# Kernel tuning notes

Measured on AMD Instinct MI355X. Metric: run time of the kernel, lower is better.

## Reference

```python
import jax, jax.numpy as jnp
import numpy as np

# Module config (matches init_kwargs)
SHAPE = (96, 128, 128)   # (D, H, W)
NUM_LAYERS = 2
K, S, P, DIL = 3, 2, 1, 1  # kernel, stride, padding, dilation (dilation=1)


def _sparse_maxpool(feat, mask):
    """One SparseMaxPool3d layer on a densified sparse tensor.

    feat: [B, D, H, W, C] float, inactive sites hold dtype-min
    mask: [B, D, H, W, 1] float 0/1 activity mask
    Max is taken only over ACTIVE input sites in each window (spconv semantics);
    an output site is active iff any input in its window is active.
    """
    neg = jnp.finfo(feat.dtype).min
    window = (1, K, K, K, 1)
    strides = (1, S, S, S, 1)
    pad = [(0, 0), (P, P), (P, P), (P, P), (0, 0)]
    masked = jnp.where(mask > 0, feat, neg)
    pooled = jax.lax.reduce_window(masked, neg, jax.lax.max, window, strides, pad)
    mask_out = jax.lax.reduce_window(mask, jnp.array(0, feat.dtype).item() * 0.0,
                                     jax.lax.max, window, strides, pad)
    return pooled, mask_out


def setup_inputs() -> dict:
    key = jax.random.key(0)
    k1, k2, k3, k4, k5 = jax.random.split(key, 5)
    N, C, B = 200000, 32, 2
    D, H, W = SHAPE
    features = jax.random.normal(k1, (N, C), dtype=jnp.float32)
    b = jax.random.randint(k2, (N,), 0, B)
    z = jax.random.randint(k3, (N,), 0, D)
    y = jax.random.randint(k4, (N,), 0, H)
    x = jax.random.randint(k5, (N,), 0, W)
    coors = jnp.stack([b, z, y, x], axis=1).astype(jnp.int32)
    return {"features": features, "coors": coors, "batch_size": B}


def reference(features, coors, batch_size):
    D, H, W = SHAPE
    C = features.shape[1]
    b, z, y, x = coors[:, 0], coors[:, 1], coors[:, 2], coors[:, 3]
    neg = jnp.finfo(features.dtype).min
    # Densify the sparse tensor (duplicate coords resolved by max, inactive = -inf)
    dense = jnp.full((batch_size, D, H, W, C), neg, features.dtype)
    dense = dense.at[b, z, y, x].max(features)
    mask = jnp.zeros((batch_size, D, H, W, 1), features.dtype).at[b, z, y, x].set(1.0)
    for _ in range(NUM_LAYERS):
        dense, mask = _sparse_maxpool(dense, mask)
    # Equivalent of SparseConvTensor.dense(): inactive output sites are 0
    return jnp.where(mask > 0, dense, jnp.zeros((), features.dtype))
```

## Files before the change

### kernel.cpp

```cpp
#include <hip/hip_runtime.h>
#include <cfloat>
#include <cstdint>

#define B_    2
#define OD    24
#define OH    32
#define OW    32
#define NC    32
#define NBINS (B_ * OD * OH * OW)
#define RSTRIDE 16
#define OVF_CAP 100000
#define SCAN_T 1024
#define CHUNK  (NBINS / SCAN_T)

#define TZ 4
#define TY 4
#define TX 4
#define TCELLS (TZ*TY*TX)
#define NTZ (OD/TZ)
#define NTY (OH/TY)
#define NTX (OW/TX)
#define NTILES (B_*NTZ*NTY*NTX)
#define NBZ (TZ+1)
#define NBY (TY+1)
#define NBX (TX+1)
#define NB  (NBZ*NBY*NBX)
#define LIST_CAP 1792

__device__ __forceinline__ unsigned xform(float f) {
    unsigned u = __float_as_uint(f);
    return u ^ ((unsigned)((int)u >> 31) | 0x80000000u);
}
__device__ __forceinline__ float unxform(unsigned t) {
    return (t == 0u) ? 0.0f
           : __uint_as_float((t >> 31) ? (t ^ 0x80000000u) : ~t);
}

__device__ __forceinline__ void slow_apply(unsigned* sm_out, const float* feat,
                                           int rec, int fm, int cb) {
    unsigned idx = ((unsigned)rec) >> 8;
    for (int c2 = 0; c2 < NC; ++c2) {
        unsigned tvv = xform(feat[idx * NC + c2]);
#pragma unroll
        for (int k = 0; k < 8; ++k) {
            const int koff = ((k & 1) * (TY * TX) + ((k >> 1) & 1) * TX
                           + ((k >> 2) & 1)) * NC;
            if ((fm >> k) & 1) atomicMax(&sm_out[cb * NC + koff + c2], tvv);
        }
    }
}


__global__ __launch_bounds__(256) void k_bin(const int* __restrict__ coors,
                                             int* __restrict__ counts,
                                             int* __restrict__ records,
                                             int* __restrict__ ovf_n,
                                             int2* __restrict__ ovf, int N) {
    int i = blockIdx.x * blockDim.x + threadIdx.x;
    if (i >= N) return;
    int4 cc = reinterpret_cast<const int4*>(coors)[i];
    int bin = (((cc.x * OD + (cc.y >> 2)) * OH + (cc.z >> 2)) * OW + (cc.w >> 2));
    int mask = 0xFF;
    if (!(cc.y & 3)) mask &= 0x55;
    if (!(cc.z & 3)) mask &= 0x33;
    if (!(cc.w & 3)) mask &= 0x0F;
    int rec = (i << 8) | mask;
    int pos = atomicAdd(&counts[bin], 1);
    if (pos < RSTRIDE) {
        records[bin * RSTRIDE + pos] = rec;
    } else {
        int o = atomicAdd(ovf_n, 1);
        if (o < OVF_CAP) ovf[o] = make_int2(bin, rec);
    }
}


__global__ __launch_bounds__(512) void k_tile(const float* __restrict__ feat,
                                              const int* __restrict__ counts,
                                              const int* __restrict__ records,
                                              const int* __restrict__ ovf_n,
                                              const int2* __restrict__ ovf,
                                              float4* __restrict__ out4) {
    __shared__ unsigned sm_out[TCELLS * NC];
    __shared__ int2 list[LIST_CAP];
    __shared__ int sm_cursor;

    const int t   = (blockIdx.x & 7) * (NTILES / 8) + (blockIdx.x >> 3);
    const int tid = threadIdx.x;
    const int tx_ = t & (NTX - 1);
    const int ty_ = (t >> 3) & (NTY - 1);
    const int rest = t >> 6;
    const int b   = (rest >= NTZ) ? 1 : 0;
    const int tz_ = rest - b * NTZ;
    const int tz0 = tz_ * TZ, ty0 = ty_ * TY, tx0 = tx_ * TX;

    if (tid == 0) sm_cursor = 0;
    for (int v = tid; v < TCELLS * NC; v += 512) sm_out[v] = 0u;
    __syncthreads();

    if (tid < 4 * NB) {
        int bn  = tid >> 2;
        int sl  = tid & 3;
        int rz  = bn / (NBY * NBX);
        int rem = bn - rz * (NBY * NBX);
        int ry  = rem / NBX;
        int rx  = rem - ry * NBX;
        int bz = tz0 - 1 + rz, by = ty0 - 1 + ry, bx = tx0 - 1 + rx;
        if ((bz | by | bx) >= 0) {
            int bin = ((b * OD + bz) * OH + by) * OW + bx;
            int cnt = counts[bin]; if (cnt > RSTRIDE) cnt = RSTRIDE;
            int4 q = *(const int4*)(records + bin * RSTRIDE + sl * 4);
            int bi = rz - 1, bj = ry - 1, bl = rx - 1;
            int vm = 0xFF;
            if (bi < 0) vm &= 0xAA;  if (bi > TZ - 2) vm &= 0x55;
            if (bj < 0) vm &= 0xCC;  if (bj > TY - 2) vm &= 0x33;
            if (bl < 0) vm &= 0xF0;  if (bl > TX - 2) vm &= 0x0F;
            int cb = bi * (TY * TX) + bj * TX + bl;
            int rs0 = sl << 2;
            int f0 = (rs0 + 0 < cnt) ? (q.x & vm & 0xFF) : 0;
            int f1 = (rs0 + 1 < cnt) ? (q.y & vm & 0xFF) : 0;
            int f2 = (rs0 + 2 < cnt) ? (q.z & vm & 0xFF) : 0;
            int f3 = (rs0 + 3 < cnt) ? (q.w & vm & 0xFF) : 0;
            int nk = (f0 != 0) + (f1 != 0) + (f2 != 0) + (f3 != 0);
            if (nk) {
                int pos = atomicAdd(&sm_cursor, nk);
                if (f0) { if (pos < LIST_CAP) list[pos] = make_int2((q.x & ~0xFF) | f0, cb);
                          else slow_apply(sm_out, feat, q.x, f0, cb); ++pos; }
                if (f1) { if (pos < LIST_CAP) list[pos] = make_int2((q.y & ~0xFF) | f1, cb);
                          else slow_apply(sm_out, feat, q.y, f1, cb); ++pos; }
                if (f2) { if (pos < LIST_CAP) list[pos] = make_int2((q.z & ~0xFF) | f2, cb);
                          else slow_apply(sm_out, feat, q.z, f2, cb); ++pos; }
                if (f3) { if (pos < LIST_CAP) list[pos] = make_int2((q.w & ~0xFF) | f3, cb);
                          else slow_apply(sm_out, feat, q.w, f3, cb); ++pos; }
            }
        }
    }

    int on = *ovf_n;
    if (on > 0 && tid == 0) {
        if (on > OVF_CAP) on = OVF_CAP;
        for (int e = 0; e < on; ++e) {
            int2 ov = ovf[e];
            int bx = ov.x & (OW - 1);
            int by = (ov.x >> 5) & (OH - 1);
            int rest2 = ov.x >> 10;
            int bb = (rest2 >= OD) ? 1 : 0;
            int bz = rest2 - bb * OD;
            if (bb != b) continue;
            int rz = bz - (tz0 - 1), ry = by - (ty0 - 1), rx = bx - (tx0 - 1);
            if (rz < 0 || rz >= NBZ || ry < 0 || ry >= NBY || rx < 0 || rx >= NBX) continue;
            int bi = rz - 1, bj = ry - 1, bl = rx - 1;
            int vm = 0xFF;
            if (bi < 0) vm &= 0xAA;  if (bi > TZ - 2) vm &= 0x55;
            if (bj < 0) vm &= 0xCC;  if (bj > TY - 2) vm &= 0x33;
            if (bl < 0) vm &= 0xF0;  if (bl > TX - 2) vm &= 0x0F;
            int fm = ov.y & vm & 0xFF;
            if (fm) {
                int pos = atomicAdd(&sm_cursor, 1);
                if (pos < LIST_CAP)
                    list[pos] = make_int2((ov.y & ~0xFF) | fm,
                                          bi * (TY * TX) + bj * TX + bl);
            }
        }
    }
    __syncthreads();
    int total = sm_cursor; if (total > LIST_CAP) total = LIST_CAP;

    const int s = tid >> 5;
    const int c = tid & 31;

    for (int j0 = s; j0 < total; j0 += 128) {
        int2 e[8];
        unsigned tv[8];
#pragma unroll
        for (int u = 0; u < 8; ++u) {
            int j = j0 + 16 * u;
            e[u] = (j < total) ? list[j] : make_int2(0, 0);
        }
#pragma unroll
        for (int u = 0; u < 8; ++u)
            tv[u] = xform(feat[(((unsigned)e[u].x) >> 8) * NC + c]);
#pragma unroll
        for (int u = 0; u < 8; ++u) {
#pragma unroll
            for (int k = 0; k < 8; ++k) {
                const int koff = ((k & 1) * (TY * TX) + ((k >> 1) & 1) * TX
                               + ((k >> 2) & 1)) * NC + c;
                if ((e[u].x >> k) & 1) atomicMax(&sm_out[e[u].y * NC + koff], tv[u]);
            }
        }
    }
    __syncthreads();

    {
        const int cell = tid >> 3, quad = tid & 7;
        const int i = cell >> 4, jj = (cell >> 2) & 3, l = cell & 3;
        uint4 uv = *(const uint4*)&sm_out[cell * NC + quad * 4];
        float4 o;
        o.x = unxform(uv.x); o.y = unxform(uv.y);
        o.z = unxform(uv.z); o.w = unxform(uv.w);
        out4[(((size_t)(b * OD + tz0 + i) * OH + (ty0 + jj)) * OW
              + (tx0 + l)) * (NC / 4) + quad] = o;
    }
}


__global__ void k_hist(const int* __restrict__ coors, int* __restrict__ counts, int N) {
    int i = blockIdx.x * blockDim.x + threadIdx.x;
    if (i >= N) return;
    int4 cc = reinterpret_cast<const int4*>(coors)[i];
    int bin = (((cc.x * OD + (cc.y >> 2)) * OH + (cc.z >> 2)) * OW + (cc.w >> 2));
    atomicAdd(&counts[bin], 1);
}

__global__ void k_scan(const int* __restrict__ counts,
                       int2* __restrict__ binfo,
                       int* __restrict__ cursor) {
    __shared__ int lds[SCAN_T];
    int t = threadIdx.x;
    int base = t * CHUNK;
    int s = 0;
#pragma unroll
    for (int k = 0; k < CHUNK; ++k) s += counts[base + k];
    lds[t] = s;
    __syncthreads();
    for (int d = 1; d < SCAN_T; d <<= 1) {
        int v = (t >= d) ? lds[t - d] : 0;
        __syncthreads();
        lds[t] += v;
        __syncthreads();
    }
    int excl = (t == 0) ? 0 : lds[t - 1];
    for (int k = 0; k < CHUNK; ++k) {
        int i = base + k;
        int c = counts[i];
        binfo[i] = make_int2(excl, c);
        cursor[i] = excl;
        excl += c;
    }
}

__global__ void k_place(const int* __restrict__ coors, int* __restrict__ cursor,
                        int* __restrict__ records, int N) {
    int i = blockIdx.x * blockDim.x + threadIdx.x;
    if (i >= N) return;
    int4 cc = reinterpret_cast<const int4*>(coors)[i];
    int bin = (((cc.x * OD + (cc.y >> 2)) * OH + (cc.z >> 2)) * OW + (cc.w >> 2));
    int pos = atomicAdd(&cursor[bin], 1);
    records[pos] = (i << 6) | (cc.y & 3) | ((cc.z & 3) << 2) | ((cc.w & 3) << 4);
}

__global__ __launch_bounds__(256) void k_gather_fb(const float4* __restrict__ feat4,
                                                   const int2* __restrict__ binfo,
                                                   const int* __restrict__ records,
                                                   float4* __restrict__ out4, int N) {
    int tid  = blockIdx.x * blockDim.x + threadIdx.x;
    int wid  = tid >> 6;
    int lane = threadIdx.x & 63;
    int q    = lane >> 3;
    int cq   = lane & 7;

    int ox  = wid & (OW - 1);
    int oy  = (wid >> 5) & (OH - 1);
    int bzc = wid >> 10;
    int b   = (bzc >= OD) ? 1 : 0;
    int oz  = bzc - b * OD;

    int2 bi[8];
#pragma unroll
    for (int k = 0; k < 8; ++k) {
        const int lz = k & 1, ly = (k >> 1) & 1, lx = (k >> 2) & 1;
        int z2 = oz - lz, y2 = oy - ly, x2 = ox - lx;
        bool okbin = ((z2 | y2 | x2) >= 0);
        int bin = ((b * OD + z2) * OH + y2) * OW + x2;
        int2 v = binfo[okbin ? bin : 0];
        if (!okbin) { v.x = N; v.y = 0; }
        bi[k] = v;
    }

    int recs[8];
#pragma unroll
    for (int k = 0; k < 8; ++k) {
        int j = (q < bi[k].y) ? q : 0;
        recs[k] = records[bi[k].x + j];
    }

    float4 m = make_float4(-FLT_MAX, -FLT_MAX, -FLT_MAX, -FLT_MAX);
    int any = 0;
#pragma unroll
    for (int k = 0; k < 8; ++k) {
        int rec = recs[k];
        bool ok = (q < bi[k].y);
        if (k & 1) ok = ok && ((rec & 3)  != 0);
        if (k & 2) ok = ok && ((rec & 12) != 0);
        if (k & 4) ok = ok && ((rec & 48) != 0);
        if (ok) {
            float4 f = feat4[(rec >> 6) * (NC / 4) + cq];
            m.x = fmaxf(m.x, f.x); m.y = fmaxf(m.y, f.y);
            m.z = fmaxf(m.z, f.z); m.w = fmaxf(m.w, f.w);
            any = 1;
        }
    }

#pragma unroll
    for (int k = 0; k < 8; ++k) {
        for (int j0 = 8; j0 < bi[k].y; j0 += 8) {
            int j = j0 + q;
            bool ok = (j < bi[k].y);
            int rec = records[bi[k].x + (ok ? j : 0)];
            if (k & 1) ok = ok && ((rec & 3)  != 0);
            if (k & 2) ok = ok && ((rec & 12) != 0);
            if (k & 4) ok = ok && ((rec & 48) != 0);
            if (ok) {
                float4 f = feat4[(rec >> 6) * (NC / 4) + cq];
                m.x = fmaxf(m.x, f.x); m.y = fmaxf(m.y, f.y);
                m.z = fmaxf(m.z, f.z); m.w = fmaxf(m.w, f.w);
                any = 1;
            }
        }
    }

#pragma unroll
    for (int s = 8; s < 64; s <<= 1) {
        m.x = fmaxf(m.x, __shfl_xor(m.x, s, 64));
        m.y = fmaxf(m.y, __shfl_xor(m.y, s, 64));
        m.z = fmaxf(m.z, __shfl_xor(m.z, s, 64));
        m.w = fmaxf(m.w, __shfl_xor(m.w, s, 64));
    }
    bool active = (__ballot(any) != 0ULL);

    if (q == 0) {
        float4 z4 = make_float4(0.f, 0.f, 0.f, 0.f);
        out4[wid * (NC / 4) + cq] = active ? m : z4;
    }
}


extern "C" void kernel_launch(void* const* d_in, const int* in_sizes, int n_in,
                              void* d_out, int out_size, void* d_ws, size_t ws_size,
                              hipStream_t stream) {
    const float* feat  = (const float*)d_in[0];
    const int*   coors = (const int*)d_in[1];
    const int N = in_sizes[0] / NC;
    float* out = (float*)d_out;

    const size_t fast_ints = (size_t)NBINS + 8 + (size_t)NBINS * RSTRIDE
                           + 2ull * OVF_CAP;
    if (ws_size >= fast_ints * sizeof(int)) {
        int*  counts  = (int*)d_ws;
        int*  ovf_n   = counts + NBINS;
        int*  records = counts + NBINS + 8;
        int2* ovf     = (int2*)(records + (size_t)NBINS * RSTRIDE);

        hipMemsetAsync(counts, 0, (NBINS + 8) * sizeof(int), stream);
        k_bin<<<(N + 255) / 256, 256, 0, stream>>>(coors, counts, records,
                                                   ovf_n, ovf, N);
        k_tile<<<NTILES, 512, 0, stream>>>(feat, counts, records,
                                           ovf_n, (const int2*)ovf, (float4*)out);
    } else {
        int*  counts  = (int*)d_ws;
        int2* binfo   = (int2*)(counts + NBINS);
        int*  cursor  = (int*)(binfo + NBINS);
        int*  records = cursor + NBINS;

        hipMemsetAsync(counts, 0, NBINS * sizeof(int), stream);
        k_hist <<<(N + 255) / 256, 256, 0, stream>>>(coors, counts, N);
        k_scan <<<1, SCAN_T, 0, stream>>>(counts, binfo, cursor);
        k_place<<<(N + 255) / 256, 256, 0, stream>>>(coors, cursor, records, N);
        k_gather_fb<<<(NBINS * 64) / 256, 256, 0, stream>>>(
            (const float4*)feat, (const int2*)binfo, records, (float4*)out, N);
    }
}
```

Baseline: 41.26 us.

## Replace shared atomicMax scatter with per-cell index lists and register max gather

Rewrites the tile kernel's inner phase. Each input record is now expanded into per-output-cell index lists in shared memory (with a small shared overflow list) instead of one shared list with bitmasks. Each thread then computes the max for four cells over one channel in registers, replacing the per-channel shared atomicMax scatter and the float/uint ordering transform. The trade is more shared atomics during list building and uneven per-cell loop lengths in the gather phase.

```diff
diff --git a/kernel.cpp b/kernel.cpp
--- a/kernel.cpp
+++ b/kernel.cpp
@@ -16,7 +16,7 @@
 #define TZ 4
 #define TY 4
 #define TX 4
-#define TCELLS (TZ*TY*TX)
+#define TCELLS 64
 #define NTZ (OD/TZ)
 #define NTY (OH/TY)
 #define NTX (OW/TX)
@@ -25,30 +25,8 @@
 #define NBY (TY+1)
 #define NBX (TX+1)
 #define NB  (NBZ*NBY*NBX)
-#define LIST_CAP 1792
-
-__device__ __forceinline__ unsigned xform(float f) {
-    unsigned u = __float_as_uint(f);
-    return u ^ ((unsigned)((int)u >> 31) | 0x80000000u);
-}
-__device__ __forceinline__ float unxform(unsigned t) {
-    return (t == 0u) ? 0.0f
-           : __uint_as_float((t >> 31) ? (t ^ 0x80000000u) : ~t);
-}
-
-__device__ __forceinline__ void slow_apply(unsigned* sm_out, const float* feat,
-                                           int rec, int fm, int cb) {
-    unsigned idx = ((unsigned)rec) >> 8;
-    for (int c2 = 0; c2 < NC; ++c2) {
-        unsigned tvv = xform(feat[idx * NC + c2]);
-#pragma unroll
-        for (int k = 0; k < 8; ++k) {
-            const int koff = ((k & 1) * (TY * TX) + ((k >> 1) & 1) * TX
-                           + ((k >> 2) & 1)) * NC;
-            if ((fm >> k) & 1) atomicMax(&sm_out[cb * NC + koff + c2], tvv);
-        }
-    }
-}
+#define CELLCAP 64
+#define SOVF_CAP 1024
 
 
 __global__ __launch_bounds__(256) void k_bin(const int* __restrict__ coors,
@@ -74,16 +52,31 @@
     }
 }
 
+__device__ __forceinline__ void push_rec(int rec, int fm, int cb,
+                                         int* cellcnt, int* celllist,
+                                         int2* sovf, int* sovf_n) {
+    int idx = (int)(((unsigned)rec) >> 8);
+    while (fm) {
+        int k = __builtin_ctz(fm); fm &= fm - 1;
+        int cell = cb + ((k & 1) << 4) + (((k >> 1) & 1) << 2) + ((k >> 2) & 1);
+        int pos = atomicAdd(&cellcnt[cell], 1);
+        if (pos < CELLCAP) celllist[cell * CELLCAP + pos] = idx;
+        else { int o = atomicAdd(sovf_n, 1);
+               if (o < SOVF_CAP) sovf[o] = make_int2(cell, idx); }
+    }
+}
+
 
 __global__ __launch_bounds__(512) void k_tile(const float* __restrict__ feat,
                                               const int* __restrict__ counts,
                                               const int* __restrict__ records,
                                               const int* __restrict__ ovf_n,
                                               const int2* __restrict__ ovf,
-                                              float4* __restrict__ out4) {
-    __shared__ unsigned sm_out[TCELLS * NC];
-    __shared__ int2 list[LIST_CAP];
-    __shared__ int sm_cursor;
+                                              float* __restrict__ out) {
+    __shared__ int  cellcnt[TCELLS];
+    __shared__ int  celllist[TCELLS * CELLCAP];
+    __shared__ int2 sovf[SOVF_CAP];
+    __shared__ int  sovf_n;
 
     const int t   = (blockIdx.x & 7) * (NTILES / 8) + (blockIdx.x >> 3);
     const int tid = threadIdx.x;
@@ -94,8 +87,8 @@
     const int tz_ = rest - b * NTZ;
     const int tz0 = tz_ * TZ, ty0 = ty_ * TY, tx0 = tx_ * TX;
 
-    if (tid == 0) sm_cursor = 0;
-    for (int v = tid; v < TCELLS * NC; v += 512) sm_out[v] = 0u;
+    if (tid < TCELLS) cellcnt[tid] = 0;
+    if (tid == 0) sovf_n = 0;
     __syncthreads();
 
     if (tid < 4 * NB) {
@@ -121,18 +114,10 @@
             int f1 = (rs0 + 1 < cnt) ? (q.y & vm & 0xFF) : 0;
             int f2 = (rs0 + 2 < cnt) ? (q.z & vm & 0xFF) : 0;
             int f3 = (rs0 + 3 < cnt) ? (q.w & vm & 0xFF) : 0;
-            int nk = (f0 != 0) + (f1 != 0) + (f2 != 0) + (f3 != 0);
-            if (nk) {
-                int pos = atomicAdd(&sm_cursor, nk);
-                if (f0) { if (pos < LIST_CAP) list[pos] = make_int2((q.x & ~0xFF) | f0, cb);
-                          else slow_apply(sm_out, feat, q.x, f0, cb); ++pos; }
-                if (f1) { if (pos < LIST_CAP) list[pos] = make_int2((q.y & ~0xFF) | f1, cb);
-                          else slow_apply(sm_out, feat, q.y, f1, cb); ++pos; }
-                if (f2) { if (pos < LIST_CAP) list[pos] = make_int2((q.z & ~0xFF) | f2, cb);
-                          else slow_apply(sm_out, feat, q.z, f2, cb); ++pos; }
-                if (f3) { if (pos < LIST_CAP) list[pos] = make_int2((q.w & ~0xFF) | f3, cb);
-                          else slow_apply(sm_out, feat, q.w, f3, cb); ++pos; }
-            }
+            if (f0) push_rec(q.x, f0, cb, cellcnt, celllist, sovf, &sovf_n);
+            if (f1) push_rec(q.y, f1, cb, cellcnt, celllist, sovf, &sovf_n);
+            if (f2) push_rec(q.z, f2, cb, cellcnt, celllist, sovf, &sovf_n);
+            if (f3) push_rec(q.w, f3, cb, cellcnt, celllist, sovf, &sovf_n);
         }
     }
 
@@ -155,53 +140,59 @@
             if (bj < 0) vm &= 0xCC;  if (bj > TY - 2) vm &= 0x33;
             if (bl < 0) vm &= 0xF0;  if (bl > TX - 2) vm &= 0x0F;
             int fm = ov.y & vm & 0xFF;
-            if (fm) {
-                int pos = atomicAdd(&sm_cursor, 1);
-                if (pos < LIST_CAP)
-                    list[pos] = make_int2((ov.y & ~0xFF) | fm,
-                                          bi * (TY * TX) + bj * TX + bl);
-            }
+            if (fm) push_rec(ov.y, fm, bi * (TY * TX) + bj * TX + bl,
+                             cellcnt, celllist, sovf, &sovf_n);
         }
     }
     __syncthreads();
-    int total = sm_cursor; if (total > LIST_CAP) total = LIST_CAP;
-
-    const int s = tid >> 5;
-    const int c = tid & 31;
-
-    for (int j0 = s; j0 < total; j0 += 128) {
-        int2 e[8];
-        unsigned tv[8];
-#pragma unroll
-        for (int u = 0; u < 8; ++u) {
-            int j = j0 + 16 * u;
-            e[u] = (j < total) ? list[j] : make_int2(0, 0);
-        }
-#pragma unroll
-        for (int u = 0; u < 8; ++u)
-            tv[u] = xform(feat[(((unsigned)e[u].x) >> 8) * NC + c]);
-#pragma unroll
-        for (int u = 0; u < 8; ++u) {
-#pragma unroll
-            for (int k = 0; k < 8; ++k) {
-                const int koff = ((k & 1) * (TY * TX) + ((k >> 1) & 1) * TX
-                               + ((k >> 2) & 1)) * NC + c;
-                if ((e[u].x >> k) & 1) atomicMax(&sm_out[e[u].y * NC + koff], tv[u]);
-            }
-        }
-    }
-    __syncthreads();
-
-    {
-        const int cell = tid >> 3, quad = tid & 7;
-        const int i = cell >> 4, jj = (cell >> 2) & 3, l = cell & 3;
-        uint4 uv = *(const uint4*)&sm_out[cell * NC + quad * 4];
-        float4 o;
-        o.x = unxform(uv.x); o.y = unxform(uv.y);
-        o.z = unxform(uv.z); o.w = unxform(uv.w);
-        out4[(((size_t)(b * OD + tz0 + i) * OH + (ty0 + jj)) * OW
-              + (tx0 + l)) * (NC / 4) + quad] = o;
-    }
+
+    const int cg = tid >> 5;
+    const int ch = tid & 31;
+    float m0 = -FLT_MAX, m1 = -FLT_MAX, m2 = -FLT_MAX, m3 = -FLT_MAX;
+    int n0, n1, n2, n3;
+
+#define GATHER(MV, NV, CELL) do {                                           \
+    int nn = cellcnt[CELL]; NV = nn; if (nn > CELLCAP) nn = CELLCAP;        \
+    const int* L = &celllist[(CELL) * CELLCAP];                             \
+    for (int j = 0; j < nn; j += 4) {                                       \
+        int4 iq = *(const int4*)&L[j];                                      \
+        int i1 = (j + 1 < nn) ? iq.y : iq.x;   \
+        int i2 = (j + 2 < nn) ? iq.z : iq.x;                                \
+        int i3 = (j + 3 < nn) ? iq.w : iq.x;                                \
+        float f0 = feat[(unsigned)iq.x * NC + ch];                          \
+        float f1 = feat[(unsigned)i1 * NC + ch];                            \
+        float f2 = feat[(unsigned)i2 * NC + ch];                            \
+        float f3 = feat[(unsigned)i3 * NC + ch];                            \
+        MV = fmaxf(MV, fmaxf(fmaxf(f0, f1), fmaxf(f2, f3)));                \
+    } } while (0)
+
+    GATHER(m0, n0, cg * 4 + 0);
+    GATHER(m1, n1, cg * 4 + 1);
+    GATHER(m2, n2, cg * 4 + 2);
+    GATHER(m3, n3, cg * 4 + 3);
+#undef GATHER
+
+    int son = sovf_n; if (son > SOVF_CAP) son = SOVF_CAP;
+    for (int j = 0; j < son; ++j) {
+        int2 e = sovf[j];
+        float f = feat[(unsigned)e.y * NC + ch];
+        if (e.x == cg * 4 + 0) m0 = fmaxf(m0, f);
+        else if (e.x == cg * 4 + 1) m1 = fmaxf(m1, f);
+        else if (e.x == cg * 4 + 2) m2 = fmaxf(m2, f);
+        else if (e.x == cg * 4 + 3) m3 = fmaxf(m3, f);
+    }
+
+#define WRITE(MV, NV, CELL) do {                                            \
+    int iz = (CELL) >> 4, iy = ((CELL) >> 2) & 3, ix = (CELL) & 3;          \
+    size_t o = ((((size_t)(b * OD + tz0 + iz)) * OH + (ty0 + iy)) * OW      \
+               + (tx0 + ix)) * NC + ch;                                     \
+    out[o] = (NV > 0) ? MV : 0.0f; } while (0)
+
+    WRITE(m0, n0, cg * 4 + 0);
+    WRITE(m1, n1, cg * 4 + 1);
+    WRITE(m2, n2, cg * 4 + 2);
+    WRITE(m3, n3, cg * 4 + 3);
+#undef WRITE
 }
 
 
@@ -356,7 +347,7 @@
         k_bin<<<(N + 255) / 256, 256, 0, stream>>>(coors, counts, records,
                                                    ovf_n, ovf, N);
         k_tile<<<NTILES, 512, 0, stream>>>(feat, counts, records,
-                                           ovf_n, (const int2*)ovf, (float4*)out);
+                                           ovf_n, (const int2*)ovf, out);
     } else {
         int*  counts  = (int*)d_ws;
         int2* binfo   = (int2*)(counts + NBINS);
```

After: 43.04 us. 1.04x slower.
